# Optimization experiments

Measured on AMD Instinct MI355X. Metric: run time of the kernel, lower is better.

The kernel has to match this reference:

```python
import jax, jax.numpy as jnp
import numpy as np

K = 1024          # num_embeddings
D = 256           # embedding_dim
COMMIT = 0.1      # commitment_cost
EPS = float(np.finfo(np.float32).eps)


def setup_inputs() -> dict:
    key = jax.random.key(0)
    k1, k2 = jax.random.split(key)
    X = jax.random.normal(k1, (16, 4096, D), dtype=jnp.float32)
    # matches nn.Embedding init: uniform(-1/K, 1/K)
    emb_weight = jax.random.uniform(k2, (K, D), dtype=jnp.float32,
                                    minval=-1.0 / K, maxval=1.0 / K)
    return {"X": X, "emb_weight": emb_weight}


def reference(X, emb_weight):
    B, N, Dm = X.shape
    Xf = X.reshape(-1, Dm)                                  # [BN, D]
    dist = (jnp.sum(Xf * Xf, axis=-1, keepdims=True)
            + jnp.sum(emb_weight * emb_weight, axis=-1)
            - 2.0 * Xf @ emb_weight.T)                      # [BN, K]
    idx = jnp.argmin(dist, axis=-1)                         # [BN]
    # one-hot @ codebook == gather
    quantized = emb_weight[idx].reshape(X.shape)            # [B, N, D]
    # perplexity from one-hot mean == normalized counts
    counts = jnp.zeros((K,), dtype=X.dtype).at[idx].add(1.0)
    avg_probs = counts / Xf.shape[0]
    perplexity = jnp.exp(-jnp.sum(avg_probs * jnp.log(avg_probs + EPS)))
    # vq loss (learnable codebook branch)
    sg = jax.lax.stop_gradient
    e_latent = jnp.mean((sg(quantized) - X) ** 2)
    q_latent = jnp.mean((quantized - sg(X)) ** 2)
    loss_vq = q_latent + COMMIT * e_latent
    # straight-through estimator
    quantized_st = X + sg(quantized - X)
    encoding_indices = idx.reshape(B, N)
    return quantized_st, encoding_indices, perplexity, loss_vq
```

## Files before the change

### kernel.cpp

```cpp
#include <hip/hip_runtime.h>
#include <math.h>

#define ROWS 65536
#define DIM  256
#define KC   1024
#define NQ   (ROWS * DIM)


__device__ __forceinline__ float sq_sum_numpy(const float* __restrict__ p) {
    float halves[2];
#pragma unroll
    for (int h = 0; h < 2; ++h) {
        const float* a = p + h * 128;
        float4 u0 = *(const float4*)(a);
        float4 u1 = *(const float4*)(a + 4);
        float r0 = __fmul_rn(u0.x, u0.x);
        float r1 = __fmul_rn(u0.y, u0.y);
        float r2 = __fmul_rn(u0.z, u0.z);
        float r3 = __fmul_rn(u0.w, u0.w);
        float r4 = __fmul_rn(u1.x, u1.x);
        float r5 = __fmul_rn(u1.y, u1.y);
        float r6 = __fmul_rn(u1.z, u1.z);
        float r7 = __fmul_rn(u1.w, u1.w);
        for (int i = 8; i < 128; i += 8) {
            float4 v0 = *(const float4*)(a + i);
            float4 v1 = *(const float4*)(a + i + 4);
            r0 = __fadd_rn(r0, __fmul_rn(v0.x, v0.x));
            r1 = __fadd_rn(r1, __fmul_rn(v0.y, v0.y));
            r2 = __fadd_rn(r2, __fmul_rn(v0.z, v0.z));
            r3 = __fadd_rn(r3, __fmul_rn(v0.w, v0.w));
            r4 = __fadd_rn(r4, __fmul_rn(v1.x, v1.x));
            r5 = __fadd_rn(r5, __fmul_rn(v1.y, v1.y));
            r6 = __fadd_rn(r6, __fmul_rn(v1.z, v1.z));
            r7 = __fadd_rn(r7, __fmul_rn(v1.w, v1.w));
        }
        float s01 = __fadd_rn(r0, r1);
        float s23 = __fadd_rn(r2, r3);
        float s45 = __fadd_rn(r4, r5);
        float s67 = __fadd_rn(r6, r7);
        halves[h] = __fadd_rn(__fadd_rn(s01, s23), __fadd_rn(s45, s67));
    }
    return __fadd_rn(halves[0], halves[1]);
}

__global__ __launch_bounds__(256) void k_prepB(const float* __restrict__ E,
                                               float* __restrict__ B32) {
    int j = blockIdx.x * 256 + threadIdx.x;
    if (j >= KC) return;
    B32[j] = sq_sum_numpy(E + (size_t)j * DIM);
}

__global__ __launch_bounds__(256) void k_prepA(const float* __restrict__ X,
                                               float* __restrict__ Arr) {
    int r = blockIdx.x * 256 + threadIdx.x;
    Arr[r] = sq_sum_numpy(X + (size_t)r * DIM);
}

#define TM 128
#define TN 128
#define TD 32
#define LSTR 132

__global__ __launch_bounds__(256) void k_pass1(
    const float* __restrict__ X, const float* __restrict__ E,
    const float* __restrict__ B32, const float* __restrict__ Arr,
    int* __restrict__ idx32)
{
    __shared__ float sm[2 * TD * LSTR];
    float* Xs = sm;
    float* Es = sm + TD * LSTR;

    const int tid = threadIdx.x;
    const int tx = tid & 15;
    const int ty = tid >> 4;
    const int rowbase = blockIdx.x * TM;

    float a8[8];
#pragma unroll
    for (int i = 0; i < 8; ++i) a8[i] = Arr[rowbase + ty * 8 + i];

    float v1[8]; int i1[8];
#pragma unroll
    for (int i = 0; i < 8; ++i) { v1[i] = 3.0e38f; i1[i] = 0; }

    for (int cb = 0; cb < KC; cb += TN) {
        float acc[8][8];
#pragma unroll
        for (int i = 0; i < 8; ++i)
#pragma unroll
            for (int j = 0; j < 8; ++j) acc[i][j] = 0.0f;

        for (int dc = 0; dc < DIM; dc += TD) {
            __syncthreads();
#pragma unroll
            for (int k = 0; k < 4; ++k) {
                int fi  = tid + k * 256;
                int r   = fi >> 3;
                int dd4 = (fi & 7) * 4;
                float4 xv = *(const float4*)(X + (size_t)(rowbase + r) * DIM + dc + dd4);
                Xs[(dd4 + 0) * LSTR + r] = xv.x;
                Xs[(dd4 + 1) * LSTR + r] = xv.y;
                Xs[(dd4 + 2) * LSTR + r] = xv.z;
                Xs[(dd4 + 3) * LSTR + r] = xv.w;
                float4 ev = *(const float4*)(E + (size_t)(cb + r) * DIM + dc + dd4);
                Es[(dd4 + 0) * LSTR + r] = ev.x;
                Es[(dd4 + 1) * LSTR + r] = ev.y;
                Es[(dd4 + 2) * LSTR + r] = ev.z;
                Es[(dd4 + 3) * LSTR + r] = ev.w;
            }
            __syncthreads();

#pragma unroll 8
            for (int dd = 0; dd < TD; ++dd) {
                float xr[8], er[8];
                float4 t0 = *(float4*)&Xs[dd * LSTR + ty * 8];
                float4 t1 = *(float4*)&Xs[dd * LSTR + ty * 8 + 4];
                xr[0]=t0.x; xr[1]=t0.y; xr[2]=t0.z; xr[3]=t0.w;
                xr[4]=t1.x; xr[5]=t1.y; xr[6]=t1.z; xr[7]=t1.w;
                float4 u0 = *(float4*)&Es[dd * LSTR + tx * 8];
                float4 u1 = *(float4*)&Es[dd * LSTR + tx * 8 + 4];
                er[0]=u0.x; er[1]=u0.y; er[2]=u0.z; er[3]=u0.w;
                er[4]=u1.x; er[5]=u1.y; er[6]=u1.z; er[7]=u1.w;
#pragma unroll
                for (int i = 0; i < 8; ++i)
#pragma unroll
                    for (int j = 0; j < 8; ++j)
                        acc[i][j] = fmaf(xr[i], er[j], acc[i][j]);
            }
        }

#pragma unroll
        for (int j = 0; j < 8; ++j) {
            int c = cb + tx * 8 + j;
            float b = B32[c];
#pragma unroll
            for (int i = 0; i < 8; ++i) {
                float Cv = __fmul_rn(2.0f, acc[i][j]);
                float t1v = __fadd_rn(a8[i], b);
                float dv  = __fsub_rn(t1v, Cv);
                if (dv < v1[i]) { v1[i] = dv; i1[i] = c; }
            }
        }
    }

    __syncthreads();
    float* Mv = sm;
    int*   Mi = (int*)(sm + 2048);
#pragma unroll
    for (int i = 0; i < 8; ++i) {
        int r = ty * 8 + i;
        Mv[r * 16 + tx] = v1[i];
        Mi[r * 16 + tx] = i1[i];
    }
    __syncthreads();
    if (tid < TM) {
        int r = tid;
        float bv = Mv[r * 16];
        int   bi = Mi[r * 16];
        for (int t = 1; t < 16; ++t) {
            float av = Mv[r * 16 + t];
            int   ai = Mi[r * 16 + t];
            if (av < bv || (av == bv && ai < bi)) { bv = av; bi = ai; }
        }
        idx32[rowbase + r] = bi;
    }
}

__global__ __launch_bounds__(256) void k_out(
    const float* __restrict__ X, const float* __restrict__ E,
    const int* __restrict__ idx32, float* __restrict__ out0,
    double* __restrict__ lossacc)
{
    const int NF4 = NQ / 4;
    double s = 0.0;
    for (int g = blockIdx.x * blockDim.x + threadIdx.x; g < NF4;
         g += gridDim.x * blockDim.x) {
        int row = g >> 6;
        int d4  = g & 63;
        int j = idx32[row];
        float4 q = *(const float4*)(E + (size_t)j * DIM + d4 * 4);
        float4 x = *(const float4*)(X + (size_t)g * 4);
        *(float4*)(out0 + (size_t)g * 4) = q;
        double dx;
        dx = (double)q.x - (double)x.x; s = fma(dx, dx, s);
        dx = (double)q.y - (double)x.y; s = fma(dx, dx, s);
        dx = (double)q.z - (double)x.z; s = fma(dx, dx, s);
        dx = (double)q.w - (double)x.w; s = fma(dx, dx, s);
    }
#pragma unroll
    for (int off = 32; off > 0; off >>= 1) s += __shfl_down(s, off, 64);
    __shared__ double wsum[4];
    int lane = threadIdx.x & 63, wv = threadIdx.x >> 6;
    if (lane == 0) wsum[wv] = s;
    __syncthreads();
    if (threadIdx.x == 0) {
        double t = wsum[0] + wsum[1] + wsum[2] + wsum[3];
        atomicAdd(lossacc, t);
    }
}

__global__ __launch_bounds__(256) void k_idxout(
    const int* __restrict__ idx32, float* __restrict__ out1,
    int* __restrict__ counts)
{
    __shared__ int h[KC];
    for (int i = threadIdx.x; i < KC; i += 256) h[i] = 0;
    __syncthreads();
    int r = blockIdx.x * 256 + threadIdx.x;
    int j = idx32[r];
    out1[r] = (float)j;
    atomicAdd(&h[j], 1);
    __syncthreads();
    for (int i = threadIdx.x; i < KC; i += 256)
        if (h[i]) atomicAdd(&counts[i], h[i]);
}

__global__ void k_fin(const int* __restrict__ counts,
                      const double* __restrict__ lossacc,
                      float* __restrict__ out_pl)
{
    __shared__ double sh[256];
    double s = 0.0;
    for (int i = threadIdx.x; i < KC; i += 256) {
        double p = (double)counts[i] / 65536.0;
        s += p * log(p + 1.1920928955078125e-07);
    }
    sh[threadIdx.x] = s;
    __syncthreads();
    for (int off = 128; off > 0; off >>= 1) {
        if (threadIdx.x < off) sh[threadIdx.x] += sh[threadIdx.x + off];
        __syncthreads();
    }
    if (threadIdx.x == 0) {
        out_pl[0] = (float)exp(-sh[0]);
        out_pl[1] = (float)((*lossacc / (double)NQ) * 1.1);
    }
}

extern "C" void kernel_launch(void* const* d_in, const int* in_sizes, int n_in,
                              void* d_out, int out_size, void* d_ws, size_t ws_size,
                              hipStream_t stream) {
    const float* X = (const float*)d_in[0];
    const float* E = (const float*)d_in[1];
    float* out = (float*)d_out;
    char* ws = (char*)d_ws;

    double* lossacc = (double*)(ws + 0);
    int*    counts  = (int*)(ws + 16);
    float*  B32     = (float*)(ws + 4224);
    float*  Arr     = (float*)(ws + 8320);
    int*    idx32   = (int*)(ws + 270464);

    hipMemsetAsync(d_ws, 0, 4224, stream);

    hipLaunchKernelGGL(k_prepB, dim3(4),        dim3(256), 0, stream, E, B32);
    hipLaunchKernelGGL(k_prepA, dim3(256),      dim3(256), 0, stream, X, Arr);
    hipLaunchKernelGGL(k_pass1, dim3(ROWS / TM), dim3(256), 0, stream,
                       X, E, B32, Arr, idx32);
    hipLaunchKernelGGL(k_out,   dim3(2048),     dim3(256), 0, stream,
                       X, E, idx32, out, lossacc);
    hipLaunchKernelGGL(k_idxout, dim3(256),     dim3(256), 0, stream,
                       idx32, out + NQ, counts);
    hipLaunchKernelGGL(k_fin,   dim3(1),        dim3(256), 0, stream,
                       counts, lossacc, out + NQ + 65536);
}
```

Baseline: 597.8 us.

## Double-buffer pass1 shared tiles with register prefetch, XOR swizzle, fuse row norms

Restructures the distance GEMM kernel to double-buffer the X and E shared-memory tiles. The global loads for the next tile go into registers while the current tile is computed, which removes one barrier per step. The shared layout changes from a padded stride to an XOR swizzle to avoid bank conflicts, and the codebook-norm loads are vectorised. The separate row-norm kernel is folded into pass1, with two threads per row computing half sums. The kernel also requests two blocks per CU through launch bounds. This raises register pressure and doubles shared memory use.

```diff
diff --git a/kernel.cpp b/kernel.cpp
--- a/kernel.cpp
+++ b/kernel.cpp
@@ -7,40 +7,40 @@
 #define NQ   (ROWS * DIM)
 
 
+__device__ __forceinline__ float half_sq_sum(const float* __restrict__ a) {
+    float4 u0 = *(const float4*)(a);
+    float4 u1 = *(const float4*)(a + 4);
+    float r0 = __fmul_rn(u0.x, u0.x);
+    float r1 = __fmul_rn(u0.y, u0.y);
+    float r2 = __fmul_rn(u0.z, u0.z);
+    float r3 = __fmul_rn(u0.w, u0.w);
+    float r4 = __fmul_rn(u1.x, u1.x);
+    float r5 = __fmul_rn(u1.y, u1.y);
+    float r6 = __fmul_rn(u1.z, u1.z);
+    float r7 = __fmul_rn(u1.w, u1.w);
+    for (int i = 8; i < 128; i += 8) {
+        float4 v0 = *(const float4*)(a + i);
+        float4 v1 = *(const float4*)(a + i + 4);
+        r0 = __fadd_rn(r0, __fmul_rn(v0.x, v0.x));
+        r1 = __fadd_rn(r1, __fmul_rn(v0.y, v0.y));
+        r2 = __fadd_rn(r2, __fmul_rn(v0.z, v0.z));
+        r3 = __fadd_rn(r3, __fmul_rn(v0.w, v0.w));
+        r4 = __fadd_rn(r4, __fmul_rn(v1.x, v1.x));
+        r5 = __fadd_rn(r5, __fmul_rn(v1.y, v1.y));
+        r6 = __fadd_rn(r6, __fmul_rn(v1.z, v1.z));
+        r7 = __fadd_rn(r7, __fmul_rn(v1.w, v1.w));
+    }
+    float s01 = __fadd_rn(r0, r1);
+    float s23 = __fadd_rn(r2, r3);
+    float s45 = __fadd_rn(r4, r5);
+    float s67 = __fadd_rn(r6, r7);
+    return __fadd_rn(__fadd_rn(s01, s23), __fadd_rn(s45, s67));
+}
+
 __device__ __forceinline__ float sq_sum_numpy(const float* __restrict__ p) {
-    float halves[2];
-#pragma unroll
-    for (int h = 0; h < 2; ++h) {
-        const float* a = p + h * 128;
-        float4 u0 = *(const float4*)(a);
-        float4 u1 = *(const float4*)(a + 4);
-        float r0 = __fmul_rn(u0.x, u0.x);
-        float r1 = __fmul_rn(u0.y, u0.y);
-        float r2 = __fmul_rn(u0.z, u0.z);
-        float r3 = __fmul_rn(u0.w, u0.w);
-        float r4 = __fmul_rn(u1.x, u1.x);
-        float r5 = __fmul_rn(u1.y, u1.y);
-        float r6 = __fmul_rn(u1.z, u1.z);
-        float r7 = __fmul_rn(u1.w, u1.w);
-        for (int i = 8; i < 128; i += 8) {
-            float4 v0 = *(const float4*)(a + i);
-            float4 v1 = *(const float4*)(a + i + 4);
-            r0 = __fadd_rn(r0, __fmul_rn(v0.x, v0.x));
-            r1 = __fadd_rn(r1, __fmul_rn(v0.y, v0.y));
-            r2 = __fadd_rn(r2, __fmul_rn(v0.z, v0.z));
-            r3 = __fadd_rn(r3, __fmul_rn(v0.w, v0.w));
-            r4 = __fadd_rn(r4, __fmul_rn(v1.x, v1.x));
-            r5 = __fadd_rn(r5, __fmul_rn(v1.y, v1.y));
-            r6 = __fadd_rn(r6, __fmul_rn(v1.z, v1.z));
-            r7 = __fadd_rn(r7, __fmul_rn(v1.w, v1.w));
-        }
-        float s01 = __fadd_rn(r0, r1);
-        float s23 = __fadd_rn(r2, r3);
-        float s45 = __fadd_rn(r4, r5);
-        float s67 = __fadd_rn(r6, r7);
-        halves[h] = __fadd_rn(__fadd_rn(s01, s23), __fadd_rn(s45, s67));
-    }
-    return __fadd_rn(halves[0], halves[1]);
+    float h0 = half_sq_sum(p);
+    float h1 = half_sq_sum(p + 128);
+    return __fadd_rn(h0, h1);
 }
 
 __global__ __launch_bounds__(256) void k_prepB(const float* __restrict__ E,
@@ -50,93 +50,136 @@
     B32[j] = sq_sum_numpy(E + (size_t)j * DIM);
 }
 
-__global__ __launch_bounds__(256) void k_prepA(const float* __restrict__ X,
-                                               float* __restrict__ Arr) {
-    int r = blockIdx.x * 256 + threadIdx.x;
-    Arr[r] = sq_sum_numpy(X + (size_t)r * DIM);
-}
-
 #define TM 128
 #define TN 128
 #define TD 32
-#define LSTR 132
-
-__global__ __launch_bounds__(256) void k_pass1(
+#define BUFF 4096
+#define BSTR 8192
+
+__global__ __launch_bounds__(256, 2) void k_pass1(
     const float* __restrict__ X, const float* __restrict__ E,
-    const float* __restrict__ B32, const float* __restrict__ Arr,
-    int* __restrict__ idx32)
+    const float* __restrict__ B32, int* __restrict__ idx32)
 {
-    __shared__ float sm[2 * TD * LSTR];
-    float* Xs = sm;
-    float* Es = sm + TD * LSTR;
+    __shared__ __align__(16) float sm[2 * BSTR];
 
     const int tid = threadIdx.x;
-    const int tx = tid & 15;
-    const int ty = tid >> 4;
+    const int tx  = tid & 15;
+    const int ty  = tid >> 4;
     const int rowbase = blockIdx.x * TM;
 
+    float4 xv0, xv1, xv2, xv3, ev0, ev1, ev2, ev3;
+
+#define LOADR(cbn, dcn)                                                         \
+    do {                                                                        \
+        int fi_, r_, d4_;                                                       \
+        fi_ = tid;       r_ = fi_ >> 3; d4_ = (fi_ & 7) << 2;                   \
+        xv0 = *(const float4*)(X + (size_t)(rowbase + r_) * DIM + (dcn) + d4_); \
+        ev0 = *(const float4*)(E + (size_t)((cbn) + r_) * DIM + (dcn) + d4_);   \
+        fi_ = tid + 256; r_ = fi_ >> 3; d4_ = (fi_ & 7) << 2;                   \
+        xv1 = *(const float4*)(X + (size_t)(rowbase + r_) * DIM + (dcn) + d4_); \
+        ev1 = *(const float4*)(E + (size_t)((cbn) + r_) * DIM + (dcn) + d4_);   \
+        fi_ = tid + 512; r_ = fi_ >> 3; d4_ = (fi_ & 7) << 2;                   \
+        xv2 = *(const float4*)(X + (size_t)(rowbase + r_) * DIM + (dcn) + d4_); \
+        ev2 = *(const float4*)(E + (size_t)((cbn) + r_) * DIM + (dcn) + d4_);   \
+        fi_ = tid + 768; r_ = fi_ >> 3; d4_ = (fi_ & 7) << 2;                   \
+        xv3 = *(const float4*)(X + (size_t)(rowbase + r_) * DIM + (dcn) + d4_); \
+        ev3 = *(const float4*)(E + (size_t)((cbn) + r_) * DIM + (dcn) + d4_);   \
+    } while (0)
+
+#define WRITE1(Xs_, Es_, v_, e_, fif_)                                          \
+    do {                                                                        \
+        int r_ = (fif_) >> 3, d4_ = ((fif_) & 7) << 2;                          \
+        int off_ = d4_ * 128 + ((((r_) >> 2) ^ (d4_ >> 2)) << 2) + ((r_) & 3);  \
+        (Xs_)[off_]       = v_.x; (Xs_)[off_ + 128] = v_.y;                     \
+        (Xs_)[off_ + 256] = v_.z; (Xs_)[off_ + 384] = v_.w;                     \
+        (Es_)[off_]       = e_.x; (Es_)[off_ + 128] = e_.y;                     \
+        (Es_)[off_ + 256] = e_.z; (Es_)[off_ + 384] = e_.w;                     \
+    } while (0)
+
+#define WRITEB(b)                                                               \
+    do {                                                                        \
+        float* Xs_ = sm + (b) * BSTR;                                           \
+        float* Es_ = Xs_ + BUFF;                                                \
+        WRITE1(Xs_, Es_, xv0, ev0, tid);                                        \
+        WRITE1(Xs_, Es_, xv1, ev1, tid + 256);                                  \
+        WRITE1(Xs_, Es_, xv2, ev2, tid + 512);                                  \
+        WRITE1(Xs_, Es_, xv3, ev3, tid + 768);                                  \
+    } while (0)
+
+    LOADR(0, 0);
+
+    {
+        int r = tid >> 1, h = tid & 1;
+        sm[(r << 1) + h] = half_sq_sum(X + (size_t)(rowbase + r) * DIM + (h << 7));
+    }
+    __syncthreads();
     float a8[8];
 #pragma unroll
-    for (int i = 0; i < 8; ++i) a8[i] = Arr[rowbase + ty * 8 + i];
+    for (int i = 0; i < 8; ++i)
+        a8[i] = __fadd_rn(sm[(ty * 8 + i) * 2], sm[(ty * 8 + i) * 2 + 1]);
+    __syncthreads();
+    WRITEB(0);
 
     float v1[8]; int i1[8];
 #pragma unroll
     for (int i = 0; i < 8; ++i) { v1[i] = 3.0e38f; i1[i] = 0; }
 
-    for (int cb = 0; cb < KC; cb += TN) {
+    int cur = 0;
+    for (int cb8 = 0; cb8 < 8; ++cb8) {
+        const int cbase = cb8 * TN;
+        float4 bq0 = *(const float4*)(B32 + cbase + (tx << 2));
+        float4 bq1 = *(const float4*)(B32 + cbase + 64 + (tx << 2));
+
         float acc[8][8];
 #pragma unroll
         for (int i = 0; i < 8; ++i)
 #pragma unroll
             for (int j = 0; j < 8; ++j) acc[i][j] = 0.0f;
 
-        for (int dc = 0; dc < DIM; dc += TD) {
+        for (int dc8 = 0; dc8 < 8; ++dc8) {
+            const int s = cb8 * 8 + dc8;
             __syncthreads();
-#pragma unroll
-            for (int k = 0; k < 4; ++k) {
-                int fi  = tid + k * 256;
-                int r   = fi >> 3;
-                int dd4 = (fi & 7) * 4;
-                float4 xv = *(const float4*)(X + (size_t)(rowbase + r) * DIM + dc + dd4);
-                Xs[(dd4 + 0) * LSTR + r] = xv.x;
-                Xs[(dd4 + 1) * LSTR + r] = xv.y;
-                Xs[(dd4 + 2) * LSTR + r] = xv.z;
-                Xs[(dd4 + 3) * LSTR + r] = xv.w;
-                float4 ev = *(const float4*)(E + (size_t)(cb + r) * DIM + dc + dd4);
-                Es[(dd4 + 0) * LSTR + r] = ev.x;
-                Es[(dd4 + 1) * LSTR + r] = ev.y;
-                Es[(dd4 + 2) * LSTR + r] = ev.z;
-                Es[(dd4 + 3) * LSTR + r] = ev.w;
+            if (s < 63) {
+                const int sn = s + 1;
+                LOADR((sn >> 3) * TN, (sn & 7) * TD);
             }
-            __syncthreads();
-
-#pragma unroll 8
-            for (int dd = 0; dd < TD; ++dd) {
-                float xr[8], er[8];
-                float4 t0 = *(float4*)&Xs[dd * LSTR + ty * 8];
-                float4 t1 = *(float4*)&Xs[dd * LSTR + ty * 8 + 4];
-                xr[0]=t0.x; xr[1]=t0.y; xr[2]=t0.z; xr[3]=t0.w;
-                xr[4]=t1.x; xr[5]=t1.y; xr[6]=t1.z; xr[7]=t1.w;
-                float4 u0 = *(float4*)&Es[dd * LSTR + tx * 8];
-                float4 u1 = *(float4*)&Es[dd * LSTR + tx * 8 + 4];
-                er[0]=u0.x; er[1]=u0.y; er[2]=u0.z; er[3]=u0.w;
-                er[4]=u1.x; er[5]=u1.y; er[6]=u1.z; er[7]=u1.w;
-#pragma unroll
-                for (int i = 0; i < 8; ++i)
-#pragma unroll
-                    for (int j = 0; j < 8; ++j)
-                        acc[i][j] = fmaf(xr[i], er[j], acc[i][j]);
+            {
+                const float* Xc = sm + cur * BSTR;
+                const float* Ec = Xc + BUFF;
+#pragma unroll 2
+                for (int dq = 0; dq < 8; ++dq) {
+                    const float* xp0 = Xc + dq * 512 + ((((ty << 1)    ) ^ dq) << 2);
+                    const float* xp1 = Xc + dq * 512 + ((((ty << 1) | 1) ^ dq) << 2);
+                    const float* ep0 = Ec + dq * 512 + ((tx ^ dq) << 2);
+#pragma unroll
+                    for (int ddi = 0; ddi < 4; ++ddi) {
+                        float4 t0 = *(const float4*)(xp0 + ddi * 128);
+                        float4 t1 = *(const float4*)(xp1 + ddi * 128);
+                        float4 u0 = *(const float4*)(ep0 + ddi * 128);
+                        float4 u1 = *(const float4*)(ep0 + ddi * 128 + 64);
+                        float xr[8] = {t0.x, t0.y, t0.z, t0.w, t1.x, t1.y, t1.z, t1.w};
+                        float er[8] = {u0.x, u0.y, u0.z, u0.w, u1.x, u1.y, u1.z, u1.w};
+#pragma unroll
+                        for (int i = 0; i < 8; ++i)
+#pragma unroll
+                            for (int j = 0; j < 8; ++j)
+                                acc[i][j] = fmaf(xr[i], er[j], acc[i][j]);
+                    }
+                }
             }
+            if (s < 63) WRITEB(cur ^ 1);
+            cur ^= 1;
         }
 
+        float bvv[8] = {bq0.x, bq0.y, bq0.z, bq0.w, bq1.x, bq1.y, bq1.z, bq1.w};
 #pragma unroll
         for (int j = 0; j < 8; ++j) {
-            int c = cb + tx * 8 + j;
-            float b = B32[c];
+            const int c = cbase + ((j < 4) ? ((tx << 2) + j)
+                                           : (64 + (tx << 2) + (j - 4)));
 #pragma unroll
             for (int i = 0; i < 8; ++i) {
-                float Cv = __fmul_rn(2.0f, acc[i][j]);
-                float t1v = __fadd_rn(a8[i], b);
+                float Cv  = __fmul_rn(2.0f, acc[i][j]);
+                float t1v = __fadd_rn(a8[i], bvv[j]);
                 float dv  = __fsub_rn(t1v, Cv);
                 if (dv < v1[i]) { v1[i] = dv; i1[i] = c; }
             }
@@ -164,6 +207,9 @@
         }
         idx32[rowbase + r] = bi;
     }
+#undef LOADR
+#undef WRITE1
+#undef WRITEB
 }
 
 __global__ __launch_bounds__(256) void k_out(
@@ -248,19 +294,17 @@
     double* lossacc = (double*)(ws + 0);
     int*    counts  = (int*)(ws + 16);
     float*  B32     = (float*)(ws + 4224);
-    float*  Arr     = (float*)(ws + 8320);
     int*    idx32   = (int*)(ws + 270464);
 
     hipMemsetAsync(d_ws, 0, 4224, stream);
 
-    hipLaunchKernelGGL(k_prepB, dim3(4),        dim3(256), 0, stream, E, B32);
-    hipLaunchKernelGGL(k_prepA, dim3(256),      dim3(256), 0, stream, X, Arr);
+    hipLaunchKernelGGL(k_prepB, dim3(4),         dim3(256), 0, stream, E, B32);
     hipLaunchKernelGGL(k_pass1, dim3(ROWS / TM), dim3(256), 0, stream,
-                       X, E, B32, Arr, idx32);
-    hipLaunchKernelGGL(k_out,   dim3(2048),     dim3(256), 0, stream,
+                       X, E, B32, idx32);
+    hipLaunchKernelGGL(k_out,   dim3(2048),      dim3(256), 0, stream,
                        X, E, idx32, out, lossacc);
-    hipLaunchKernelGGL(k_idxout, dim3(256),     dim3(256), 0, stream,
+    hipLaunchKernelGGL(k_idxout, dim3(256),      dim3(256), 0, stream,
                        idx32, out + NQ, counts);
-    hipLaunchKernelGGL(k_fin,   dim3(1),        dim3(256), 0, stream,
+    hipLaunchKernelGGL(k_fin,   dim3(1),         dim3(256), 0, stream,
                        counts, lossacc, out + NQ + 65536);
 }
```

Measured after the change: 571.1 us. 4.5% less time.
